# Kernel tuning notes

Measured on AMD Instinct MI355X. Metric: run time of the kernel, lower is better.

## Reference

```python
import jax, jax.numpy as jnp
import numpy as np

H, W, WS, KS, D, CF, HEAD = 64, 64, 8, 8, 512, 128, 8
INC = D + CF  # 640
GH, GW = H // WS, W // WS  # 8, 8
G = GH * GW  # 64 windows
NW = WS * WS  # 64 tokens per window
DH = D // HEAD  # 64


def _ln(x, g, b, eps=1e-5):
    m = jnp.mean(x, axis=-1, keepdims=True)
    v = jnp.var(x, axis=-1, keepdims=True)
    return (x - m) * jax.lax.rsqrt(v + eps) * g + b


def _lin(x, w, b):
    # torch Linear: w [out,in]
    return jnp.einsum('...i,oi->...o', x, w) + b


def _dwconv(x_nchw, w, b):
    # depthwise conv, stride=KS, VALID; w [C,1,KS,KS]
    y = jax.lax.conv_general_dilated(
        x_nchw, w, window_strides=(KS, KS), padding='VALID',
        feature_group_count=x_nchw.shape[1])
    return y + b[None, :, None, None]


def _win(x):  # [bt,H,W,c] -> [bt,G,NW,c]
    bt, _, _, c = x.shape
    x = x.reshape(bt, GH, WS, GW, WS, c).transpose(0, 1, 3, 2, 4, 5)
    return x.reshape(bt, G, NW, c)


def setup_inputs() -> dict:
    key = jax.random.key(0)
    ks = jax.random.split(key, 20)
    s = 0.02
    inp = {
        'x': jax.random.normal(ks[0], (8, H * W, D), jnp.float32),
        'f': jax.random.normal(ks[1], (8, H * W, CF), jnp.float32),
        'wq': jax.random.normal(ks[2], (D, INC), jnp.float32) * s,
        'bq': jnp.zeros((D,), jnp.float32),
        'wk': jax.random.normal(ks[3], (D, INC), jnp.float32) * s,
        'bk': jnp.zeros((D,), jnp.float32),
        'wv': jax.random.normal(ks[4], (D, D), jnp.float32) * s,
        'bv': jnp.zeros((D,), jnp.float32),
        'wo': jax.random.normal(ks[5], (D, D), jnp.float32) * s,
        'bo': jnp.zeros((D,), jnp.float32),
        'rw_w': jax.random.normal(ks[6], (INC, INC), jnp.float32) * s,
        'rw_b': jnp.zeros((INC,), jnp.float32),
        'convk_w': jax.random.normal(ks[7], (INC, 1, KS, KS), jnp.float32) * s,
        'convk_b': jnp.zeros((INC,), jnp.float32),
        'convv_w': jax.random.normal(ks[8], (D, 1, KS, KS), jnp.float32) * s,
        'convv_b': jnp.zeros((D,), jnp.float32),
        'qn_g': jnp.ones((INC,), jnp.float32), 'qn_b': jnp.zeros((INC,), jnp.float32),
        'kn_g': jnp.ones((INC,), jnp.float32), 'kn_b': jnp.zeros((INC,), jnp.float32),
        'vn_g': jnp.ones((D,), jnp.float32), 'vn_b': jnp.zeros((D,), jnp.float32),
        't': 1,
    }
    return inp


def reference(x, f, wq, bq, wk, bk, wv, bv, wo, bo, rw_w, rw_b,
              convk_w, convk_b, convv_w, convv_b,
              qn_g, qn_b, kn_g, kn_b, vn_g, vn_b, t):
    bt, n, c = x.shape
    x4 = x.reshape(bt, H, W, c)
    f4 = f.reshape(bt, H, W, CF)
    # no padding: H,W divisible by WS
    qk = jnp.concatenate([x4, f4], axis=-1)  # [bt,H,W,INC]
    qk = qk * jax.nn.sigmoid(_lin(qk, rw_w, rw_b))
    q = _win(qk)  # [bt,G,NW,INC]
    # global K tokens via depthwise strided conv
    kg = _dwconv(qk.transpose(0, 3, 1, 2), convk_w, convk_b)  # [bt,INC,GH,GW]
    kg = kg.transpose(0, 2, 3, 1).reshape(bt, 1, -1, INC)
    kg = jnp.broadcast_to(kg, (bt, G, kg.shape[2], INC))
    k = jnp.concatenate([q, kg], axis=2)  # [bt,G,NW+Ng,INC]
    q = _ln(q, qn_g, qn_b)
    k = _ln(k, kn_g, kn_b)
    # global V tokens
    vg = _dwconv(x4.transpose(0, 3, 1, 2), convv_w, convv_b)  # [bt,D,GH,GW]
    vg = vg.transpose(0, 2, 3, 1).reshape(bt, 1, -1, c)
    vg = jnp.broadcast_to(vg, (bt, G, vg.shape[2], c))
    xw = _win(x4)  # [bt,G,NW,c]
    v = _ln(jnp.concatenate([xw, vg], axis=2), vn_g, vn_b)
    # projections
    query = _lin(q, wq, bq).reshape(bt, G, NW, HEAD, DH)
    key = _lin(k, wk, bk).reshape(bt, G, -1, HEAD, DH)
    value = _lin(v, wv, bv).reshape(bt, G, -1, HEAD, DH)
    scores = jnp.einsum('bgqhd,bgkhd->bghqk', query, key) / jnp.sqrt(jnp.float32(DH))
    attn = jax.nn.softmax(scores, axis=-1)
    out = jnp.einsum('bghqk,bgkhd->bgqhd', attn, value).reshape(bt, G, NW, c)
    # window reverse
    out = out.reshape(bt, GH, GW, WS, WS, c).transpose(0, 1, 3, 2, 4, 5)
    out = out.reshape(bt, H * W, c)
    return _lin(out, wo, bo)
```

## Files before the change

kernel.cpp:

```cpp
#include <hip/hip_runtime.h>

typedef unsigned short u16;
typedef __attribute__((ext_vector_type(8))) short s8v;
typedef __attribute__((ext_vector_type(4))) short s4v;
typedef __attribute__((ext_vector_type(4))) float f4v;

#define NTOK 32768

__device__ __forceinline__ float bf2f(u16 u){
  union { unsigned int i; float f; } p; p.i = ((unsigned int)u) << 16; return p.f;
}
__device__ __forceinline__ u16 f2bf(float f){
  union { float f; unsigned int i; } p; p.f = f;
  unsigned int r = p.i + 0x7FFFu + ((p.i >> 16) & 1u);
  return (u16)(r >> 16);
}
__device__ __forceinline__ int wtok_idx(int b, int gh, int gw, int n){
  return b*4096 + (gh*8 + (n>>3))*64 + gw*8 + (n&7);
}

__global__ __launch_bounds__(256) void prep_weights(
    const float* __restrict__ rww, const float* __restrict__ wq,
    const float* __restrict__ wk,  const float* __restrict__ wv,
    const float* __restrict__ wo,  const float* __restrict__ qng,
    const float* __restrict__ kng, const float* __restrict__ vng,
    u16* __restrict__ orw, u16* __restrict__ oq, u16* __restrict__ ok,
    u16* __restrict__ ov,  u16* __restrict__ oo)
{
  int i = blockIdx.x*256 + threadIdx.x;
  if (i < 409600){ orw[i] = f2bf(rww[i]); return; }
  i -= 409600;
  if (i < 327680){ oq[i] = f2bf(wq[i] * qng[i % 640]); return; }
  i -= 327680;
  if (i < 327680){ ok[i] = f2bf(wk[i] * kng[i % 640]); return; }
  i -= 327680;
  if (i < 262144){ ov[i] = f2bf(wv[i] * vng[i & 511]); return; }
  i -= 262144;
  oo[i] = f2bf(wo[i]);
}

__global__ __launch_bounds__(256) void prep_bias(
    const float* __restrict__ wq, const float* __restrict__ bq, const float* __restrict__ qnb,
    const float* __restrict__ wk, const float* __restrict__ bk, const float* __restrict__ knb,
    const float* __restrict__ wv, const float* __restrict__ bv, const float* __restrict__ vnb,
    float* __restrict__ obq, float* __restrict__ obk, float* __restrict__ obv)
{
  int o = blockIdx.x*256 + threadIdx.x;
  int which = o >> 9;
  int oo = o & 511;
  if (which == 0){
    float s = bq[oo];
    for (int i=0;i<640;i++) s += qnb[i]*wq[oo*640+i];
    obq[oo] = s;
  } else if (which == 1){
    float s = bk[oo];
    for (int i=0;i<640;i++) s += knb[i]*wk[oo*640+i];
    obk[oo] = s;
  } else {
    float s = bv[oo];
    for (int i=0;i<512;i++) s += vnb[i]*wv[oo*512+i];
    obv[oo] = s;
  }
}

__global__ __launch_bounds__(256) void build_qk(
    const float* __restrict__ X, const float* __restrict__ F, u16* __restrict__ qkb)
{
  int idx = blockIdx.x*256 + threadIdx.x;
  int token = idx / 160;
  int c4 = (idx - token*160) * 4;
  f4v v;
  if (c4 < 512) v = *(const f4v*)(X + (size_t)token*512 + c4);
  else          v = *(const f4v*)(F + (size_t)token*128 + (c4 - 512));
  s4v o;
  #pragma unroll
  for (int j=0;j<4;j++) o[j] = (short)f2bf(v[j]);
  *(s4v*)(qkb + (size_t)token*640 + c4) = o;
}

template<int EPI>
__global__ __launch_bounds__(256, 3) void gemm_kernel(
    const u16* __restrict__ A, const u16* __restrict__ B,
    const float* __restrict__ bias,
    u16* __restrict__ outb, float* __restrict__ outf,
    const float* __restrict__ Xr, const float* __restrict__ Fr,
    int N, int K)
{
  __shared__ u16 lA[128*64];
  __shared__ u16 lB[128*64];
  const int tid = threadIdx.x;
  const int lane = tid & 63;
  const int w = tid >> 6;
  const int wm = (w >> 1) * 64;
  const int wn = (w & 1) * 64;
  const int nb = N >> 7;
  const int m0 = (blockIdx.x / nb) << 7;
  const int n0 = (blockIdx.x % nb) << 7;

  const f4v fzero = {0.f, 0.f, 0.f, 0.f};
  f4v acc[4][4];
  #pragma unroll
  for (int i=0;i<4;i++)
    #pragma unroll
    for (int j=0;j<4;j++) acc[i][j] = fzero;

  for (int k0 = 0; k0 < K; k0 += 64){
    #pragma unroll
    for (int it=0; it<4; it++){
      int s = it*256 + tid;
      int row = s >> 3, c = s & 7;
      s8v va = *(const s8v*)(A + (size_t)(m0+row)*K + k0 + c*8);
      *(s8v*)&lA[(row*8 + (c ^ (row&7)))*8] = va;
      s8v vb = *(const s8v*)(B + (size_t)(n0+row)*K + k0 + c*8);
      *(s8v*)&lB[(row*8 + (c ^ (row&7)))*8] = vb;
    }
    __syncthreads();
    #pragma unroll
    for (int kk=0; kk<2; kk++){
      const int cg = kk*4 + (lane>>4);
      s8v bfr[4];
      #pragma unroll
      for (int ni=0; ni<4; ni++){
        int col = wn + ni*16 + (lane&15);
        bfr[ni] = *(const s8v*)&lB[(col*8 + (cg ^ (col&7)))*8];
      }
      #pragma unroll
      for (int mi=0; mi<4; mi++){
        int row = wm + mi*16 + (lane&15);
        s8v afr = *(const s8v*)&lA[(row*8 + (cg ^ (row&7)))*8];
        #pragma unroll
        for (int ni=0; ni<4; ni++)
          acc[mi][ni] = __builtin_amdgcn_mfma_f32_16x16x32_bf16(afr, bfr[ni], acc[mi][ni], 0, 0, 0);
      }
    }
    __syncthreads();
  }

  #pragma unroll
  for (int mi=0; mi<4; mi++){
    #pragma unroll
    for (int ni=0; ni<4; ni++){
      const int colg = n0 + wn + ni*16 + (lane&15);
      const float bb = bias[colg];
      #pragma unroll
      for (int j=0;j<4;j++){
        const int rowg = m0 + wm + mi*16 + (lane>>4)*4 + j;
        float v = acc[mi][ni][j] + bb;
        if constexpr (EPI == 0){
          outb[(size_t)rowg*N + colg] = f2bf(v);
        } else if constexpr (EPI == 1){
          float sg = 1.f / (1.f + __expf(-v));
          float qv = (colg < 512) ? Xr[(size_t)rowg*512 + colg]
                                  : Fr[(size_t)rowg*128 + (colg - 512)];
          outb[(size_t)rowg*N + colg] = f2bf(qv * sg);
        } else {
          outf[(size_t)rowg*N + colg] = v;
        }
      }
    }
  }
}

__global__ __launch_bounds__(256) void ln_qk_kernel(const u16* __restrict__ y, u16* __restrict__ u)
{
  int token = blockIdx.x*4 + (threadIdx.x >> 6);
  int lane = threadIdx.x & 63;
  const u16* row = y + (size_t)token*640;
  float v[10], s = 0.f, s2 = 0.f;
  #pragma unroll
  for (int i=0;i<10;i++){ float x = bf2f(row[i*64+lane]); v[i]=x; s+=x; s2+=x*x; }
  #pragma unroll
  for (int m=1;m<64;m<<=1){ s += __shfl_xor(s,m); s2 += __shfl_xor(s2,m); }
  float mean = s*(1.f/640.f);
  float var = s2*(1.f/640.f) - mean*mean;
  float rstd = rsqrtf(var + 1e-5f);
  u16* ur = u + (size_t)token*640;
  #pragma unroll
  for (int i=0;i<10;i++) ur[i*64+lane] = f2bf((v[i]-mean)*rstd);
}

__global__ __launch_bounds__(256) void ln_x_kernel(const float* __restrict__ X, u16* __restrict__ uv)
{
  int token = blockIdx.x*4 + (threadIdx.x >> 6);
  int lane = threadIdx.x & 63;
  const float* row = X + (size_t)token*512;
  float v[8], s = 0.f, s2 = 0.f;
  #pragma unroll
  for (int i=0;i<8;i++){ float x = row[i*64+lane]; v[i]=x; s+=x; s2+=x*x; }
  #pragma unroll
  for (int m=1;m<64;m<<=1){ s += __shfl_xor(s,m); s2 += __shfl_xor(s2,m); }
  float mean = s*(1.f/512.f);
  float var = s2*(1.f/512.f) - mean*mean;
  float rstd = rsqrtf(var + 1e-5f);
  u16* ur = uv + (size_t)token*512;
  #pragma unroll
  for (int i=0;i<8;i++) ur[i*64+lane] = f2bf((v[i]-mean)*rstd);
}

__global__ __launch_bounds__(640) void convk_ln_kernel(
    const u16* __restrict__ qkrw, const float* __restrict__ cw,
    const float* __restrict__ cb, u16* __restrict__ u)
{
  int bg = blockIdx.x;
  int b = bg >> 6, gpos = bg & 63;
  int gh = gpos >> 3, gw = gpos & 7;
  int ch = threadIdx.x;
  int base = b*4096 + gh*8*64 + gw*8;
  float acc = cb[ch];
  #pragma unroll
  for (int r=0;r<8;r++)
    #pragma unroll
    for (int c=0;c<8;c++)
      acc += bf2f(qkrw[(size_t)(base + r*64 + c)*640 + ch]) * cw[ch*64 + r*8 + c];
  float s = acc, s2 = acc*acc;
  #pragma unroll
  for (int m=1;m<64;m<<=1){ s += __shfl_xor(s,m); s2 += __shfl_xor(s2,m); }
  __shared__ float rs[10], rs2[10];
  int wid = threadIdx.x >> 6, lane = threadIdx.x & 63;
  if (lane == 0){ rs[wid] = s; rs2[wid] = s2; }
  __syncthreads();
  float ts = 0.f, ts2 = 0.f;
  #pragma unroll
  for (int i=0;i<10;i++){ ts += rs[i]; ts2 += rs2[i]; }
  float mean = ts*(1.f/640.f);
  float var = ts2*(1.f/640.f) - mean*mean;
  float rstd = rsqrtf(var + 1e-5f);
  u[(size_t)(NTOK + bg)*640 + ch] = f2bf((acc-mean)*rstd);
}

__global__ __launch_bounds__(512) void convv_ln_kernel(
    const float* __restrict__ X, const float* __restrict__ cw,
    const float* __restrict__ cb, u16* __restrict__ uv)
{
  int bg = blockIdx.x;
  int b = bg >> 6, gpos = bg & 63;
  int gh = gpos >> 3, gw = gpos & 7;
  int ch = threadIdx.x;
  int base = b*4096 + gh*8*64 + gw*8;
  float acc = cb[ch];
  #pragma unroll
  for (int r=0;r<8;r++)
    #pragma unroll
    for (int c=0;c<8;c++)
      acc += X[(size_t)(base + r*64 + c)*512 + ch] * cw[ch*64 + r*8 + c];
  float s = acc, s2 = acc*acc;
  #pragma unroll
  for (int m=1;m<64;m<<=1){ s += __shfl_xor(s,m); s2 += __shfl_xor(s2,m); }
  __shared__ float rs[8], rs2[8];
  int wid = threadIdx.x >> 6, lane = threadIdx.x & 63;
  if (lane == 0){ rs[wid] = s; rs2[wid] = s2; }
  __syncthreads();
  float ts = 0.f, ts2 = 0.f;
  #pragma unroll
  for (int i=0;i<8;i++){ ts += rs[i]; ts2 += rs2[i]; }
  float mean = ts*(1.f/512.f);
  float var = ts2*(1.f/512.f) - mean*mean;
  float rstd = rsqrtf(var + 1e-5f);
  uv[(size_t)(NTOK + bg)*512 + ch] = f2bf((acc-mean)*rstd);
}

__global__ __launch_bounds__(256, 2) void attn_kernel(
    const u16* __restrict__ Qp, const u16* __restrict__ Kp,
    const u16* __restrict__ Vp, u16* __restrict__ Out)
{
  int blk = blockIdx.x;
  int h = blk & 7, g = (blk >> 3) & 63, b = blk >> 9;
  int gh = g >> 3, gw = g & 7;
  int tid = threadIdx.x, lane = tid & 63, wvid = tid >> 6;

  __shared__ u16 qs[64*64];
  __shared__ u16 ks[128*64];
  __shared__ u16 vt[64*128];
  __shared__ u16 ps[64*128];
  __shared__ float red[4][64];

  for (int s = tid; s < 512; s += 256){
    int row = s >> 3, c = s & 7;
    const u16* src = Qp + (size_t)wtok_idx(b,gh,gw,row)*512 + h*64 + c*8;
    *(s8v*)&qs[(row*8 + (c ^ (row&7)))*8] = *(const s8v*)src;
  }
  for (int s = tid; s < 1024; s += 256){
    int row = s >> 3, c = s & 7;
    int t = (row < 64) ? wtok_idx(b,gh,gw,row) : (NTOK + b*64 + (row-64));
    *(s8v*)&ks[(row*8 + (c ^ (row&7)))*8] = *(const s8v*)(Kp + (size_t)t*512 + h*64 + c*8);
  }
  for (int s = tid; s < 1024; s += 256){
    int tokr = s >> 3, c = s & 7;
    int t = (tokr < 64) ? wtok_idx(b,gh,gw,tokr) : (NTOK + b*64 + (tokr-64));
    s8v vv = *(const s8v*)(Vp + (size_t)t*512 + h*64 + c*8);
    #pragma unroll
    for (int j=0;j<8;j++){
      int d = c*8 + j;
      int ck = (tokr >> 3) ^ (d & 15);
      vt[d*128 + ck*8 + (tokr & 7)] = (u16)vv[j];
    }
  }
  __syncthreads();

  const f4v fzero = {0.f,0.f,0.f,0.f};
  f4v sacc[4][2];
  #pragma unroll
  for (int i=0;i<4;i++){ sacc[i][0]=fzero; sacc[i][1]=fzero; }
  #pragma unroll
  for (int kk=0; kk<2; kk++){
    const int cg = kk*4 + (lane>>4);
    s8v bfr[2];
    #pragma unroll
    for (int ni=0; ni<2; ni++){
      int col = wvid*32 + ni*16 + (lane&15);
      bfr[ni] = *(const s8v*)&ks[(col*8 + (cg ^ (col&7)))*8];
    }
    #pragma unroll
    for (int mi=0; mi<4; mi++){
      int row = mi*16 + (lane&15);
      s8v afr = *(const s8v*)&qs[(row*8 + (cg ^ (row&7)))*8];
      #pragma unroll
      for (int ni=0; ni<2; ni++)
        sacc[mi][ni] = __builtin_amdgcn_mfma_f32_16x16x32_bf16(afr, bfr[ni], sacc[mi][ni], 0,0,0);
    }
  }

  float pex[4][2][4];
  float psum[4][4];
  #pragma unroll
  for (int mi=0; mi<4; mi++){
    #pragma unroll
    for (int j=0;j<4;j++){
      float t0 = 0.f;
      #pragma unroll
      for (int ni=0; ni<2; ni++){
        float e = __expf(sacc[mi][ni][j] * 0.125f);
        pex[mi][ni][j] = e;
        t0 += e;
      }
      #pragma unroll
      for (int m=1;m<16;m<<=1) t0 += __shfl_xor(t0, m);
      psum[mi][j] = t0;
    }
  }
  if ((lane & 15) == 0){
    #pragma unroll
    for (int mi=0; mi<4; mi++)
      #pragma unroll
      for (int j=0;j<4;j++)
        red[wvid][mi*16 + (lane>>4)*4 + j] = psum[mi][j];
  }
  __syncthreads();

  #pragma unroll
  for (int mi=0; mi<4; mi++){
    #pragma unroll
    for (int j=0;j<4;j++){
      int r = mi*16 + (lane>>4)*4 + j;
      float tot = red[0][r] + red[1][r] + red[2][r] + red[3][r];
      float inv = 1.0f / tot;
      #pragma unroll
      for (int ni=0; ni<2; ni++){
        int col = wvid*32 + ni*16 + (lane&15);
        int ck = (col >> 3) ^ (r & 15);
        ps[r*128 + ck*8 + (col & 7)] = f2bf(pex[mi][ni][j] * inv);
      }
    }
  }
  __syncthreads();

  f4v oacc[4];
  #pragma unroll
  for (int i=0;i<4;i++) oacc[i] = fzero;
  #pragma unroll
  for (int kk=0; kk<4; kk++){
    int d = wvid*16 + (lane&15);
    int cg = kk*4 + (lane>>4);
    s8v bfr = *(const s8v*)&vt[(d*16 + (cg ^ (d&15)))*8];
    #pragma unroll
    for (int mi=0; mi<4; mi++){
      int r = mi*16 + (lane&15);
      s8v afr = *(const s8v*)&ps[(r*16 + (cg ^ (r&15)))*8];
      oacc[mi] = __builtin_amdgcn_mfma_f32_16x16x32_bf16(afr, bfr, oacc[mi], 0,0,0);
    }
  }
  #pragma unroll
  for (int mi=0; mi<4; mi++)
    #pragma unroll
    for (int j=0;j<4;j++){
      int q = mi*16 + (lane>>4)*4 + j;
      Out[(size_t)wtok_idx(b,gh,gw,q)*512 + h*64 + wvid*16 + (lane&15)] = f2bf(oacc[mi][j]);
    }
}

extern "C" void kernel_launch(void* const* d_in, const int* in_sizes, int n_in,
                              void* d_out, int out_size, void* d_ws, size_t ws_size,
                              hipStream_t stream)
{
  const float* X   = (const float*)d_in[0];
  const float* F   = (const float*)d_in[1];
  const float* wq  = (const float*)d_in[2];
  const float* bq  = (const float*)d_in[3];
  const float* wk  = (const float*)d_in[4];
  const float* bk  = (const float*)d_in[5];
  const float* wv  = (const float*)d_in[6];
  const float* bv  = (const float*)d_in[7];
  const float* wo  = (const float*)d_in[8];
  const float* bo  = (const float*)d_in[9];
  const float* rww = (const float*)d_in[10];
  const float* rwb = (const float*)d_in[11];
  const float* ckw = (const float*)d_in[12];
  const float* ckb = (const float*)d_in[13];
  const float* cvw = (const float*)d_in[14];
  const float* cvb = (const float*)d_in[15];
  const float* qng = (const float*)d_in[16];
  const float* qnb = (const float*)d_in[17];
  const float* kng = (const float*)d_in[18];
  const float* knb = (const float*)d_in[19];
  const float* vng = (const float*)d_in[20];
  const float* vnb = (const float*)d_in[21];
  float* OutF = (float*)d_out;

  char* ws = (char*)d_ws;
  size_t off = 0;
  auto alloc = [&](size_t bytes){
    size_t o = off; off += (bytes + 255) & ~(size_t)255; return o;
  };
  u16*   W_RW = (u16*)  (ws + alloc((size_t)640*640*2));
  u16*   W_Q  = (u16*)  (ws + alloc((size_t)512*640*2));
  u16*   W_K  = (u16*)  (ws + alloc((size_t)512*640*2));
  u16*   W_V  = (u16*)  (ws + alloc((size_t)512*512*2));
  u16*   W_O  = (u16*)  (ws + alloc((size_t)512*512*2));
  float* B_Q  = (float*)(ws + alloc(512*4));
  float* B_K  = (float*)(ws + alloc(512*4));
  float* B_V  = (float*)(ws + alloc(512*4));
  u16*   QKB  = (u16*)  (ws + alloc((size_t)NTOK*640*2));
  u16*   QKRW = (u16*)  (ws + alloc((size_t)NTOK*640*2));
  u16*   U    = (u16*)  (ws + alloc((size_t)(NTOK+512)*640*2));
  u16*   UV   = (u16*)  (ws + alloc((size_t)(NTOK+512)*512*2));
  u16*   KP   = (u16*)  (ws + alloc((size_t)(NTOK+512)*512*2));
  u16*   VP   = (u16*)  (ws + alloc((size_t)(NTOK+512)*512*2));
  (void)in_sizes; (void)n_in; (void)out_size; (void)ws_size;

  prep_weights<<<6208, 256, 0, stream>>>(rww, wq, wk, wv, wo, qng, kng, vng,
                                         W_RW, W_Q, W_K, W_V, W_O);
  prep_bias<<<6, 256, 0, stream>>>(wq, bq, qnb, wk, bk, knb, wv, bv, vnb, B_Q, B_K, B_V);
  build_qk<<<20480, 256, 0, stream>>>(X, F, QKB);

  gemm_kernel<1><<<1280, 256, 0, stream>>>(QKB, W_RW, rwb, QKRW, nullptr, X, F, 640, 640);

  ln_qk_kernel<<<8192, 256, 0, stream>>>(QKRW, U);
  ln_x_kernel<<<8192, 256, 0, stream>>>(X, UV);
  convk_ln_kernel<<<512, 640, 0, stream>>>(QKRW, ckw, ckb, U);
  convv_ln_kernel<<<512, 512, 0, stream>>>(X, cvw, cvb, UV);

  gemm_kernel<0><<<1024, 256, 0, stream>>>(U,  W_Q, B_Q, QKB, nullptr, nullptr, nullptr, 512, 640);
  gemm_kernel<0><<<1040, 256, 0, stream>>>(U,  W_K, B_K, KP,  nullptr, nullptr, nullptr, 512, 640);
  gemm_kernel<0><<<1040, 256, 0, stream>>>(UV, W_V, B_V, VP,  nullptr, nullptr, nullptr, 512, 512);

  attn_kernel<<<4096, 256, 0, stream>>>(QKB, KP, VP, QKRW);

  gemm_kernel<2><<<1024, 256, 0, stream>>>(QKRW, W_O, bo, nullptr, OutF, nullptr, nullptr, 512, 512);
}
```

Baseline: 528.0 us.

## Fuse Q/K projections, transpose V output, load GEMM tiles directly into LDS, vectorize LNs

Merges the Q and K projection GEMMs into one N=1024 GEMM that splits its output into two buffers, and writes the V projection transposed so attention can load V fragments straight from global memory. The GEMM tile loads switch to global_load_lds, placing pre-swizzled data in LDS without going through registers. The sigmoid-gate epilogue now reads the bf16 input tile instead of the fp32 X/F. The LayerNorm kernels use 16 lanes per token with vector loads. Attention drops its Q/K/V staging in shared memory, holds fragments in registers and requests occupancy 3, which adds register pressure and uncoalesced transposed V reads.

Result: faster. 500.2 us (-5.3%).

```diff
diff --git a/kernel.cpp b/kernel.cpp
--- a/kernel.cpp
+++ b/kernel.cpp
@@ -6,6 +6,7 @@
 typedef __attribute__((ext_vector_type(4))) float f4v;
 
 #define NTOK 32768
+#define TTOK 33280
 
 __device__ __forceinline__ float bf2f(u16 u){
   union { unsigned int i; float f; } p; p.i = ((unsigned int)u) << 16; return p.f;
@@ -17,6 +18,11 @@
 }
 __device__ __forceinline__ int wtok_idx(int b, int gh, int gw, int n){
   return b*4096 + (gh*8 + (n>>3))*64 + gw*8 + (n&7);
+}
+__device__ __forceinline__ void gload16(const u16* g, u16* l){
+  __builtin_amdgcn_global_load_lds(
+      (const __attribute__((address_space(1))) void*)g,
+      (__attribute__((address_space(3))) void*)l, 16, 0, 0);
 }
 
 __global__ __launch_bounds__(256) void prep_weights(
@@ -24,15 +30,15 @@
     const float* __restrict__ wk,  const float* __restrict__ wv,
     const float* __restrict__ wo,  const float* __restrict__ qng,
     const float* __restrict__ kng, const float* __restrict__ vng,
-    u16* __restrict__ orw, u16* __restrict__ oq, u16* __restrict__ ok,
+    u16* __restrict__ orw, u16* __restrict__ oqk,
     u16* __restrict__ ov,  u16* __restrict__ oo)
 {
   int i = blockIdx.x*256 + threadIdx.x;
   if (i < 409600){ orw[i] = f2bf(rww[i]); return; }
   i -= 409600;
-  if (i < 327680){ oq[i] = f2bf(wq[i] * qng[i % 640]); return; }
+  if (i < 327680){ oqk[i] = f2bf(wq[i] * qng[i % 640]); return; }
   i -= 327680;
-  if (i < 327680){ ok[i] = f2bf(wk[i] * kng[i % 640]); return; }
+  if (i < 327680){ oqk[327680 + i] = f2bf(wk[i] * kng[i % 640]); return; }
   i -= 327680;
   if (i < 262144){ ov[i] = f2bf(wv[i] * vng[i & 511]); return; }
   i -= 262144;
@@ -43,7 +49,7 @@
     const float* __restrict__ wq, const float* __restrict__ bq, const float* __restrict__ qnb,
     const float* __restrict__ wk, const float* __restrict__ bk, const float* __restrict__ knb,
     const float* __restrict__ wv, const float* __restrict__ bv, const float* __restrict__ vnb,
-    float* __restrict__ obq, float* __restrict__ obk, float* __restrict__ obv)
+    float* __restrict__ obqk, float* __restrict__ obv)
 {
   int o = blockIdx.x*256 + threadIdx.x;
   int which = o >> 9;
@@ -51,11 +57,11 @@
   if (which == 0){
     float s = bq[oo];
     for (int i=0;i<640;i++) s += qnb[i]*wq[oo*640+i];
-    obq[oo] = s;
+    obqk[oo] = s;
   } else if (which == 1){
     float s = bk[oo];
     for (int i=0;i<640;i++) s += knb[i]*wk[oo*640+i];
-    obk[oo] = s;
+    obqk[512 + oo] = s;
   } else {
     float s = bv[oo];
     for (int i=0;i<512;i++) s += vnb[i]*wv[oo*512+i];
@@ -82,8 +88,7 @@
 __global__ __launch_bounds__(256, 3) void gemm_kernel(
     const u16* __restrict__ A, const u16* __restrict__ B,
     const float* __restrict__ bias,
-    u16* __restrict__ outb, float* __restrict__ outf,
-    const float* __restrict__ Xr, const float* __restrict__ Fr,
+    u16* __restrict__ out0, u16* __restrict__ out1, float* __restrict__ outf,
     int N, int K)
 {
   __shared__ u16 lA[128*64];
@@ -96,6 +101,7 @@
   const int nb = N >> 7;
   const int m0 = (blockIdx.x / nb) << 7;
   const int n0 = (blockIdx.x % nb) << 7;
+  const int wbase = tid & ~63;
 
   const f4v fzero = {0.f, 0.f, 0.f, 0.f};
   f4v acc[4][4];
@@ -108,11 +114,9 @@
     #pragma unroll
     for (int it=0; it<4; it++){
       int s = it*256 + tid;
-      int row = s >> 3, c = s & 7;
-      s8v va = *(const s8v*)(A + (size_t)(m0+row)*K + k0 + c*8);
-      *(s8v*)&lA[(row*8 + (c ^ (row&7)))*8] = va;
-      s8v vb = *(const s8v*)(B + (size_t)(n0+row)*K + k0 + c*8);
-      *(s8v*)&lB[(row*8 + (c ^ (row&7)))*8] = vb;
+      int row = s >> 3, cc = s & 7, cs = cc ^ (row & 7);
+      gload16(A + (size_t)(m0+row)*K + k0 + cs*8, &lA[(it*256 + wbase)*8]);
+      gload16(B + (size_t)(n0+row)*K + k0 + cs*8, &lB[(it*256 + wbase)*8]);
     }
     __syncthreads();
     #pragma unroll
@@ -142,19 +146,27 @@
     for (int ni=0; ni<4; ni++){
       const int colg = n0 + wn + ni*16 + (lane&15);
       const float bb = bias[colg];
-      #pragma unroll
-      for (int j=0;j<4;j++){
-        const int rowg = m0 + wm + mi*16 + (lane>>4)*4 + j;
-        float v = acc[mi][ni][j] + bb;
-        if constexpr (EPI == 0){
-          outb[(size_t)rowg*N + colg] = f2bf(v);
-        } else if constexpr (EPI == 1){
-          float sg = 1.f / (1.f + __expf(-v));
-          float qv = (colg < 512) ? Xr[(size_t)rowg*512 + colg]
-                                  : Fr[(size_t)rowg*128 + (colg - 512)];
-          outb[(size_t)rowg*N + colg] = f2bf(qv * sg);
-        } else {
-          outf[(size_t)rowg*N + colg] = v;
+      if constexpr (EPI == 3){
+        const int rowg0 = m0 + wm + mi*16 + (lane>>4)*4;
+        s4v pk;
+        #pragma unroll
+        for (int j=0;j<4;j++) pk[j] = (short)f2bf(acc[mi][ni][j] + bb);
+        *(s4v*)(out0 + (size_t)colg*TTOK + rowg0) = pk;
+      } else {
+        #pragma unroll
+        for (int j=0;j<4;j++){
+          const int rowg = m0 + wm + mi*16 + (lane>>4)*4 + j;
+          float v = acc[mi][ni][j] + bb;
+          if constexpr (EPI == 1){
+            float sg = 1.f / (1.f + __expf(-v));
+            float qv = bf2f(A[(size_t)rowg*640 + colg]);
+            out0[(size_t)rowg*640 + colg] = f2bf(qv * sg);
+          } else if constexpr (EPI == 2){
+            outf[(size_t)rowg*512 + colg] = v;
+          } else {
+            if (colg < 512) out0[(size_t)rowg*512 + colg] = f2bf(v);
+            else            out1[(size_t)rowg*512 + (colg-512)] = f2bf(v);
+          }
         }
       }
     }
@@ -163,38 +175,58 @@
 
 __global__ __launch_bounds__(256) void ln_qk_kernel(const u16* __restrict__ y, u16* __restrict__ u)
 {
-  int token = blockIdx.x*4 + (threadIdx.x >> 6);
-  int lane = threadIdx.x & 63;
-  const u16* row = y + (size_t)token*640;
-  float v[10], s = 0.f, s2 = 0.f;
-  #pragma unroll
-  for (int i=0;i<10;i++){ float x = bf2f(row[i*64+lane]); v[i]=x; s+=x; s2+=x*x; }
-  #pragma unroll
-  for (int m=1;m<64;m<<=1){ s += __shfl_xor(s,m); s2 += __shfl_xor(s2,m); }
+  int t = blockIdx.x*16 + (threadIdx.x >> 4);
+  int l = threadIdx.x & 15;
+  const u16* row = y + (size_t)t*640;
+  s8v v[5];
+  float s = 0.f, s2 = 0.f;
+  #pragma unroll
+  for (int p=0;p<5;p++){
+    v[p] = *(const s8v*)(row + (p*16+l)*8);
+    #pragma unroll
+    for (int j=0;j<8;j++){ float x = bf2f((u16)v[p][j]); s += x; s2 += x*x; }
+  }
+  #pragma unroll
+  for (int m=1;m<16;m<<=1){ s += __shfl_xor(s,m); s2 += __shfl_xor(s2,m); }
   float mean = s*(1.f/640.f);
   float var = s2*(1.f/640.f) - mean*mean;
   float rstd = rsqrtf(var + 1e-5f);
-  u16* ur = u + (size_t)token*640;
-  #pragma unroll
-  for (int i=0;i<10;i++) ur[i*64+lane] = f2bf((v[i]-mean)*rstd);
+  u16* ur = u + (size_t)t*640;
+  #pragma unroll
+  for (int p=0;p<5;p++){
+    s8v o;
+    #pragma unroll
+    for (int j=0;j<8;j++) o[j] = (short)f2bf((bf2f((u16)v[p][j])-mean)*rstd);
+    *(s8v*)(ur + (p*16+l)*8) = o;
+  }
 }
 
 __global__ __launch_bounds__(256) void ln_x_kernel(const float* __restrict__ X, u16* __restrict__ uv)
 {
-  int token = blockIdx.x*4 + (threadIdx.x >> 6);
-  int lane = threadIdx.x & 63;
-  const float* row = X + (size_t)token*512;
-  float v[8], s = 0.f, s2 = 0.f;
-  #pragma unroll
-  for (int i=0;i<8;i++){ float x = row[i*64+lane]; v[i]=x; s+=x; s2+=x*x; }
-  #pragma unroll
-  for (int m=1;m<64;m<<=1){ s += __shfl_xor(s,m); s2 += __shfl_xor(s2,m); }
+  int t = blockIdx.x*16 + (threadIdx.x >> 4);
+  int l = threadIdx.x & 15;
+  const float* row = X + (size_t)t*512;
+  f4v v[8];
+  float s = 0.f, s2 = 0.f;
+  #pragma unroll
+  for (int p=0;p<8;p++){
+    v[p] = *(const f4v*)(row + (p*16+l)*4);
+    #pragma unroll
+    for (int j=0;j<4;j++){ float x = v[p][j]; s += x; s2 += x*x; }
+  }
+  #pragma unroll
+  for (int m=1;m<16;m<<=1){ s += __shfl_xor(s,m); s2 += __shfl_xor(s2,m); }
   float mean = s*(1.f/512.f);
   float var = s2*(1.f/512.f) - mean*mean;
   float rstd = rsqrtf(var + 1e-5f);
-  u16* ur = uv + (size_t)token*512;
-  #pragma unroll
-  for (int i=0;i<8;i++) ur[i*64+lane] = f2bf((v[i]-mean)*rstd);
+  u16* ur = uv + (size_t)t*512;
+  #pragma unroll
+  for (int p=0;p<8;p++){
+    s4v o;
+    #pragma unroll
+    for (int j=0;j<4;j++) o[j] = (short)f2bf((v[p][j]-mean)*rstd);
+    *(s4v*)(ur + (p*16+l)*4) = o;
+  }
 }
 
 __global__ __launch_bounds__(640) void convk_ln_kernel(
@@ -259,91 +291,79 @@
   uv[(size_t)(NTOK + bg)*512 + ch] = f2bf((acc-mean)*rstd);
 }
 
-__global__ __launch_bounds__(256, 2) void attn_kernel(
+__global__ __launch_bounds__(256, 3) void attn_kernel(
     const u16* __restrict__ Qp, const u16* __restrict__ Kp,
-    const u16* __restrict__ Vp, u16* __restrict__ Out)
+    const u16* __restrict__ VT, u16* __restrict__ Out)
 {
   int blk = blockIdx.x;
   int h = blk & 7, g = (blk >> 3) & 63, b = blk >> 9;
   int gh = g >> 3, gw = g & 7;
   int tid = threadIdx.x, lane = tid & 63, wvid = tid >> 6;
-
-  __shared__ u16 qs[64*64];
-  __shared__ u16 ks[128*64];
-  __shared__ u16 vt[64*128];
+  int l15 = lane & 15, lg = lane >> 4;
+
   __shared__ u16 ps[64*128];
   __shared__ float red[4][64];
 
-  for (int s = tid; s < 512; s += 256){
-    int row = s >> 3, c = s & 7;
-    const u16* src = Qp + (size_t)wtok_idx(b,gh,gw,row)*512 + h*64 + c*8;
-    *(s8v*)&qs[(row*8 + (c ^ (row&7)))*8] = *(const s8v*)src;
-  }
-  for (int s = tid; s < 1024; s += 256){
-    int row = s >> 3, c = s & 7;
-    int t = (row < 64) ? wtok_idx(b,gh,gw,row) : (NTOK + b*64 + (row-64));
-    *(s8v*)&ks[(row*8 + (c ^ (row&7)))*8] = *(const s8v*)(Kp + (size_t)t*512 + h*64 + c*8);
-  }
-  for (int s = tid; s < 1024; s += 256){
-    int tokr = s >> 3, c = s & 7;
-    int t = (tokr < 64) ? wtok_idx(b,gh,gw,tokr) : (NTOK + b*64 + (tokr-64));
-    s8v vv = *(const s8v*)(Vp + (size_t)t*512 + h*64 + c*8);
-    #pragma unroll
-    for (int j=0;j<8;j++){
-      int d = c*8 + j;
-      int ck = (tokr >> 3) ^ (d & 15);
-      vt[d*128 + ck*8 + (tokr & 7)] = (u16)vv[j];
-    }
-  }
-  __syncthreads();
+  s8v qf[4][2], kf[2][2], vf[4];
+  #pragma unroll
+  for (int mi=0; mi<4; mi++){
+    const u16* qrow = Qp + (size_t)wtok_idx(b,gh,gw, mi*16 + l15)*512 + h*64;
+    #pragma unroll
+    for (int kk=0; kk<2; kk++)
+      qf[mi][kk] = *(const s8v*)(qrow + (kk*4+lg)*8);
+  }
+  #pragma unroll
+  for (int ni=0; ni<2; ni++){
+    int kt = wvid*32 + ni*16 + l15;
+    int tok = (kt < 64) ? wtok_idx(b,gh,gw,kt) : (NTOK + b*64 + (kt-64));
+    const u16* krow = Kp + (size_t)tok*512 + h*64;
+    #pragma unroll
+    for (int kk=0; kk<2; kk++)
+      kf[ni][kk] = *(const s8v*)(krow + (kk*4+lg)*8);
+  }
+  {
+    int d = wvid*16 + l15;
+    const u16* vrow = VT + (size_t)(h*64 + d)*TTOK;
+    #pragma unroll
+    for (int c4=0; c4<4; c4++){
+      int kt0 = (c4*4+lg)*8;
+      int tok0 = (kt0 < 64) ? wtok_idx(b,gh,gw,kt0) : (NTOK + b*64 + (kt0-64));
+      vf[c4] = *(const s8v*)(vrow + tok0);
+    }
+  }
 
   const f4v fzero = {0.f,0.f,0.f,0.f};
   f4v sacc[4][2];
   #pragma unroll
   for (int i=0;i<4;i++){ sacc[i][0]=fzero; sacc[i][1]=fzero; }
   #pragma unroll
-  for (int kk=0; kk<2; kk++){
-    const int cg = kk*4 + (lane>>4);
-    s8v bfr[2];
-    #pragma unroll
-    for (int ni=0; ni<2; ni++){
-      int col = wvid*32 + ni*16 + (lane&15);
-      bfr[ni] = *(const s8v*)&ks[(col*8 + (cg ^ (col&7)))*8];
-    }
-    #pragma unroll
-    for (int mi=0; mi<4; mi++){
-      int row = mi*16 + (lane&15);
-      s8v afr = *(const s8v*)&qs[(row*8 + (cg ^ (row&7)))*8];
+  for (int kk=0; kk<2; kk++)
+    #pragma unroll
+    for (int mi=0; mi<4; mi++)
       #pragma unroll
       for (int ni=0; ni<2; ni++)
-        sacc[mi][ni] = __builtin_amdgcn_mfma_f32_16x16x32_bf16(afr, bfr[ni], sacc[mi][ni], 0,0,0);
-    }
-  }
-
-  float pex[4][2][4];
+        sacc[mi][ni] = __builtin_amdgcn_mfma_f32_16x16x32_bf16(qf[mi][kk], kf[ni][kk], sacc[mi][ni], 0,0,0);
+
   float psum[4][4];
   #pragma unroll
   for (int mi=0; mi<4; mi++){
     #pragma unroll
     for (int j=0;j<4;j++){
-      float t0 = 0.f;
-      #pragma unroll
-      for (int ni=0; ni<2; ni++){
-        float e = __expf(sacc[mi][ni][j] * 0.125f);
-        pex[mi][ni][j] = e;
-        t0 += e;
-      }
+      float e0 = __expf(sacc[mi][0][j] * 0.125f);
+      float e1 = __expf(sacc[mi][1][j] * 0.125f);
+      sacc[mi][0][j] = e0; sacc[mi][1][j] = e1;
+      float t0 = e0 + e1;
       #pragma unroll
       for (int m=1;m<16;m<<=1) t0 += __shfl_xor(t0, m);
       psum[mi][j] = t0;
     }
   }
-  if ((lane & 15) == 0){
+  if (l15 == 0){
     #pragma unroll
     for (int mi=0; mi<4; mi++)
       #pragma unroll
       for (int j=0;j<4;j++)
-        red[wvid][mi*16 + (lane>>4)*4 + j] = psum[mi][j];
+        red[wvid][mi*16 + lg*4 + j] = psum[mi][j];
   }
   __syncthreads();
 
@@ -351,14 +371,13 @@
   for (int mi=0; mi<4; mi++){
     #pragma unroll
     for (int j=0;j<4;j++){
-      int r = mi*16 + (lane>>4)*4 + j;
-      float tot = red[0][r] + red[1][r] + red[2][r] + red[3][r];
-      float inv = 1.0f / tot;
+      int r = mi*16 + lg*4 + j;
+      float inv = 1.0f / (red[0][r] + red[1][r] + red[2][r] + red[3][r]);
       #pragma unroll
       for (int ni=0; ni<2; ni++){
-        int col = wvid*32 + ni*16 + (lane&15);
+        int col = wvid*32 + ni*16 + l15;
         int ck = (col >> 3) ^ (r & 15);
-        ps[r*128 + ck*8 + (col & 7)] = f2bf(pex[mi][ni][j] * inv);
+        ps[r*128 + ck*8 + (col & 7)] = f2bf(sacc[mi][ni][j] * inv);
       }
     }
   }
@@ -368,23 +387,20 @@
   #pragma unroll
   for (int i=0;i<4;i++) oacc[i] = fzero;
   #pragma unroll
-  for (int kk=0; kk<4; kk++){
-    int d = wvid*16 + (lane&15);
-    int cg = kk*4 + (lane>>4);
-    s8v bfr = *(const s8v*)&vt[(d*16 + (cg ^ (d&15)))*8];
+  for (int c4=0; c4<4; c4++){
+    int cg = c4*4 + lg;
     #pragma unroll
     for (int mi=0; mi<4; mi++){
-      int r = mi*16 + (lane&15);
-      s8v afr = *(const s8v*)&ps[(r*16 + (cg ^ (r&15)))*8];
-      oacc[mi] = __builtin_amdgcn_mfma_f32_16x16x32_bf16(afr, bfr, oacc[mi], 0,0,0);
+      s8v afr = *(const s8v*)&ps[((mi*16 + l15)*16 + (cg ^ l15))*8];
+      oacc[mi] = __builtin_amdgcn_mfma_f32_16x16x32_bf16(afr, vf[c4], oacc[mi], 0,0,0);
     }
   }
   #pragma unroll
   for (int mi=0; mi<4; mi++)
     #pragma unroll
     for (int j=0;j<4;j++){
-      int q = mi*16 + (lane>>4)*4 + j;
-      Out[(size_t)wtok_idx(b,gh,gw,q)*512 + h*64 + wvid*16 + (lane&15)] = f2bf(oacc[mi][j]);
+      int q = mi*16 + lg*4 + j;
+      Out[(size_t)wtok_idx(b,gh,gw,q)*512 + h*64 + wvid*16 + l15] = f2bf(oacc[mi][j]);
     }
 }
 
@@ -422,38 +438,35 @@
     size_t o = off; off += (bytes + 255) & ~(size_t)255; return o;
   };
   u16*   W_RW = (u16*)  (ws + alloc((size_t)640*640*2));
-  u16*   W_Q  = (u16*)  (ws + alloc((size_t)512*640*2));
-  u16*   W_K  = (u16*)  (ws + alloc((size_t)512*640*2));
+  u16*   W_QK = (u16*)  (ws + alloc((size_t)1024*640*2));
   u16*   W_V  = (u16*)  (ws + alloc((size_t)512*512*2));
   u16*   W_O  = (u16*)  (ws + alloc((size_t)512*512*2));
-  float* B_Q  = (float*)(ws + alloc(512*4));
-  float* B_K  = (float*)(ws + alloc(512*4));
+  float* B_QK = (float*)(ws + alloc(1024*4));
   float* B_V  = (float*)(ws + alloc(512*4));
   u16*   QKB  = (u16*)  (ws + alloc((size_t)NTOK*640*2));
   u16*   QKRW = (u16*)  (ws + alloc((size_t)NTOK*640*2));
-  u16*   U    = (u16*)  (ws + alloc((size_t)(NTOK+512)*640*2));
-  u16*   UV   = (u16*)  (ws + alloc((size_t)(NTOK+512)*512*2));
-  u16*   KP   = (u16*)  (ws + alloc((size_t)(NTOK+512)*512*2));
-  u16*   VP   = (u16*)  (ws + alloc((size_t)(NTOK+512)*512*2));
+  u16*   U    = (u16*)  (ws + alloc((size_t)TTOK*640*2));
+  u16*   UV   = (u16*)  (ws + alloc((size_t)TTOK*512*2));
+  u16*   KP   = (u16*)  (ws + alloc((size_t)TTOK*512*2));
+  u16*   VT   = (u16*)  (ws + alloc((size_t)512*TTOK*2));
   (void)in_sizes; (void)n_in; (void)out_size; (void)ws_size;
 
   prep_weights<<<6208, 256, 0, stream>>>(rww, wq, wk, wv, wo, qng, kng, vng,
-                                         W_RW, W_Q, W_K, W_V, W_O);
-  prep_bias<<<6, 256, 0, stream>>>(wq, bq, qnb, wk, bk, knb, wv, bv, vnb, B_Q, B_K, B_V);
+                                         W_RW, W_QK, W_V, W_O);
+  prep_bias<<<6, 256, 0, stream>>>(wq, bq, qnb, wk, bk, knb, wv, bv, vnb, B_QK, B_V);
   build_qk<<<20480, 256, 0, stream>>>(X, F, QKB);
 
-  gemm_kernel<1><<<1280, 256, 0, stream>>>(QKB, W_RW, rwb, QKRW, nullptr, X, F, 640, 640);
-
-  ln_qk_kernel<<<8192, 256, 0, stream>>>(QKRW, U);
-  ln_x_kernel<<<8192, 256, 0, stream>>>(X, UV);
+  gemm_kernel<1><<<1280, 256, 0, stream>>>(QKB, W_RW, rwb, QKRW, nullptr, nullptr, 640, 640);
+
+  ln_qk_kernel<<<2048, 256, 0, stream>>>(QKRW, U);
+  ln_x_kernel<<<2048, 256, 0, stream>>>(X, UV);
   convk_ln_kernel<<<512, 640, 0, stream>>>(QKRW, ckw, ckb, U);
   convv_ln_kernel<<<512, 512, 0, stream>>>(X, cvw, cvb, UV);
 
-  gemm_kernel<0><<<1024, 256, 0, stream>>>(U,  W_Q, B_Q, QKB, nullptr, nullptr, nullptr, 512, 640);
-  gemm_kernel<0><<<1040, 256, 0, stream>>>(U,  W_K, B_K, KP,  nullptr, nullptr, nullptr, 512, 640);
-  gemm_kernel<0><<<1040, 256, 0, stream>>>(UV, W_V, B_V, VP,  nullptr, nullptr, nullptr, 512, 512);
-
-  attn_kernel<<<4096, 256, 0, stream>>>(QKB, KP, VP, QKRW);
-
-  gemm_kernel<2><<<1024, 256, 0, stream>>>(QKRW, W_O, bo, nullptr, OutF, nullptr, nullptr, 512, 512);
-}
+  gemm_kernel<4><<<2080, 256, 0, stream>>>(U,  W_QK, B_QK, QKB, KP, nullptr, 1024, 640);
+  gemm_kernel<3><<<1040, 256, 0, stream>>>(UV, W_V,  B_V,  VT,  nullptr, nullptr, 512, 512);
+
+  attn_kernel<<<4096, 256, 0, stream>>>(QKB, KP, VT, QKRW);
+
+  gemm_kernel<2><<<1024, 256, 0, stream>>>(QKRW, W_O, bo, nullptr, nullptr, OutF, 512, 512);
+}
```
